# Kernel tuning notes

Hardware: AMD Instinct MI355X
Metric: run time of the kernel (lower is better)

Reference implementation:

```python
import jax, jax.numpy as jnp
import numpy as np

TEMPERATURE = 0.07
EPS = 1e-8
B, D, C = 4096, 512, 10


def setup_inputs() -> dict:
    key = jax.random.key(0)
    k1, k2 = jax.random.split(key)
    features = jax.random.normal(k1, (B, D), dtype=jnp.float32)
    cls = jax.random.randint(k2, (B,), 0, C)
    labels = jax.nn.one_hot(cls, C, dtype=jnp.float32)  # [B, C] one-hot
    return {"features": features, "labels": labels}


def reference(features, labels):
    b = features.shape[0]
    # L2-normalize rows
    feats = features / jnp.linalg.norm(features, axis=1, keepdims=True)
    sim = jnp.clip(feats @ feats.T / TEMPERATURE, -20.0, 20.0)  # [B, B]
    eye = jnp.eye(b, dtype=bool)
    sim = jnp.where(eye, -jnp.inf, sim)  # mask self-similarity

    labels_norm = labels / (labels.sum(axis=1, keepdims=True) + EPS)
    label_sim = labels_norm @ labels_norm.T  # [B, B]
    label_sim = jnp.where(eye, 0.0, label_sim)
    pos_mask = label_sim > 0.1  # [B, B] bool

    exp_sim = jnp.exp(sim)  # diag -> exp(-inf) = 0
    pos_sum = jnp.sum(jnp.where(pos_mask, exp_sim, 0.0), axis=1)  # [B]
    all_sum = jnp.sum(exp_sim, axis=1)  # diag already zero => off-diagonal sum
    loss_i = -jnp.log(pos_sum / (all_sum + EPS) + EPS)  # [B]

    valid = jnp.any(pos_mask, axis=1)  # rows with >=1 positive
    n_valid = jnp.sum(valid.astype(jnp.float32))
    total = jnp.sum(jnp.where(valid, loss_i, 0.0))
    return jnp.where(n_valid > 0, total / n_valid, 0.0)
```

## Files before the change

kernel.cpp:

```cpp
#include <hip/hip_runtime.h>


#define B_ROWS 4096
#define D_DIM  512
#define C_CLS  10
#define NTB    32
#define NTILES (NTB * (NTB + 1) / 2)

typedef __bf16 bf16x8 __attribute__((ext_vector_type(8)));
typedef float  f32x4  __attribute__((ext_vector_type(4)));

__device__ __forceinline__ void load_lds16(const __bf16* g, __bf16* l) {
  __builtin_amdgcn_global_load_lds(
      (const __attribute__((address_space(1))) unsigned int*)g,
      (__attribute__((address_space(3))) unsigned int*)l, 16, 0, 0);
}

__global__ __launch_bounds__(256) void prep_kernel(
    const float* __restrict__ feats, const float* __restrict__ labels,
    __bf16* __restrict__ F, int* __restrict__ cls,
    float* __restrict__ totals) {
  const int w = threadIdx.x >> 6, lane = threadIdx.x & 63;
  const int row = blockIdx.x * 4 + w;
  const float* fr = feats + (size_t)row * D_DIM;
  float4 v0 = ((const float4*)fr)[2 * lane];
  float4 v1 = ((const float4*)fr)[2 * lane + 1];
  float ss = v0.x*v0.x + v0.y*v0.y + v0.z*v0.z + v0.w*v0.w
           + v1.x*v1.x + v1.y*v1.y + v1.z*v1.z + v1.w*v1.w;
  #pragma unroll
  for (int m = 1; m < 64; m <<= 1) ss += __shfl_xor(ss, m, 64);
  float inv = 1.0f / sqrtf(ss);

  bf16x8 o;
  o[0] = (__bf16)(v0.x * inv); o[1] = (__bf16)(v0.y * inv);
  o[2] = (__bf16)(v0.z * inv); o[3] = (__bf16)(v0.w * inv);
  o[4] = (__bf16)(v1.x * inv); o[5] = (__bf16)(v1.y * inv);
  o[6] = (__bf16)(v1.z * inv); o[7] = (__bf16)(v1.w * inv);
  *(bf16x8*)(F + (size_t)row * D_DIM + 8 * lane) = o;

  float lv = (lane < C_CLS) ? labels[(size_t)row * C_CLS + lane] : 0.f;
  unsigned long long m = __ballot(lv > 0.5f);
  if (lane == 0) cls[row] = (int)(__ffsll((long long)m) - 1);
  if (blockIdx.x == 0 && threadIdx.x == 0) { totals[0] = 0.f; totals[1] = 0.f; }
}

__global__ __launch_bounds__(256) void sim_kernel(
    const __bf16* __restrict__ F, const int* __restrict__ cls,
    float* __restrict__ P_all, float* __restrict__ P_pos) {
  __shared__ __align__(16) __bf16 Abuf[128 * 64];
  __shared__ __align__(16) __bf16 Bbuf[128 * 64];
  __shared__ int clsA[128], clsB[128];
  __shared__ float g_row_all[128], g_row_pos[128];
  __shared__ float g_col_all[128], g_col_pos[128];

  int rem = blockIdx.x, bi = 0, rowlen = NTB;
  while (rem >= rowlen) { rem -= rowlen; ++bi; --rowlen; }
  const int bj = bi + rem;
  const int i0 = bi * 128, j0 = bj * 128;
  const bool offdiag = (bi != bj);

  const int t = threadIdx.x;
  const int w = t >> 6, lane = t & 63;
  const int wi = w & 1, wj = w >> 1;
  const int q = lane >> 4, cl = lane & 15;

  if (t < 128) { clsA[t] = cls[i0 + t]; g_row_all[t] = 0.f; g_row_pos[t] = 0.f; }
  else { clsB[t-128] = cls[j0 + t - 128]; g_col_all[t-128] = 0.f; g_col_pos[t-128] = 0.f; }

  f32x4 acc[4][4];
  #pragma unroll
  for (int ri = 0; ri < 4; ++ri)
    #pragma unroll
    for (int cj = 0; cj < 4; ++cj) acc[ri][cj] = (f32x4){0.f, 0.f, 0.f, 0.f};

  const int srow = lane >> 3;
  const int sg   = (lane & 7) ^ srow;

  for (int k0 = 0; k0 < D_DIM; k0 += 64) {
    __syncthreads();
    #pragma unroll
    for (int r = 0; r < 4; ++r) {
      const int rowbase = w * 32 + r * 8;
      load_lds16(F + (size_t)(i0 + rowbase + srow) * D_DIM + k0 + sg * 8,
                 &Abuf[rowbase * 64]);
      load_lds16(F + (size_t)(j0 + rowbase + srow) * D_DIM + k0 + sg * 8,
                 &Bbuf[rowbase * 64]);
    }
    __syncthreads();

    #pragma unroll
    for (int kk = 0; kk < 64; kk += 32) {
      const int cc = ((kk >> 3) + q) ^ (cl & 7);
      bf16x8 af[4], bfr[4];
      #pragma unroll
      for (int ri = 0; ri < 4; ++ri)
        af[ri] = *(const bf16x8*)&Abuf[(64 * wi + 16 * ri + cl) * 64 + cc * 8];
      #pragma unroll
      for (int cj = 0; cj < 4; ++cj)
        bfr[cj] = *(const bf16x8*)&Bbuf[(64 * wj + 16 * cj + cl) * 64 + cc * 8];
      #pragma unroll
      for (int ri = 0; ri < 4; ++ri)
        #pragma unroll
        for (int cj = 0; cj < 4; ++cj)
          acc[ri][cj] = __builtin_amdgcn_mfma_f32_16x16x32_bf16(
              af[ri], bfr[cj], acc[ri][cj], 0, 0, 0);
    }
  }

  const float invT = 1.0f / 0.07f;
  float cs_all[4] = {0.f, 0.f, 0.f, 0.f};
  float cs_pos[4] = {0.f, 0.f, 0.f, 0.f};

  #pragma unroll
  for (int ri = 0; ri < 4; ++ri) {
    float ra[4] = {0.f, 0.f, 0.f, 0.f};
    float rp[4] = {0.f, 0.f, 0.f, 0.f};
    #pragma unroll
    for (int cj = 0; cj < 4; ++cj) {
      const int jloc = 64 * wj + 16 * cj + cl;
      const int gj = j0 + jloc;
      const int cjc = clsB[jloc];
      #pragma unroll
      for (int r = 0; r < 4; ++r) {
        const int iloc = 64 * wi + 16 * ri + q * 4 + r;
        const int gi = i0 + iloc;
        float s = acc[ri][cj][r] * invT;
        s = fminf(fmaxf(s, -20.f), 20.f);
        const bool diag = (gi == gj);
        float e = diag ? 0.f : __expf(s);
        ra[r] += e;
        cs_all[cj] += e;
        if (!diag && cjc == clsA[iloc]) { rp[r] += e; cs_pos[cj] += e; }
      }
    }
    #pragma unroll
    for (int r = 0; r < 4; ++r) {
      float sa = ra[r], sp = rp[r];
      #pragma unroll
      for (int m = 1; m < 16; m <<= 1) {
        sa += __shfl_xor(sa, m, 64);
        sp += __shfl_xor(sp, m, 64);
      }
      if (cl == 0) {
        const int rloc = 64 * wi + 16 * ri + q * 4 + r;
        atomicAdd(&g_row_all[rloc], sa);
        atomicAdd(&g_row_pos[rloc], sp);
      }
    }
  }
  if (offdiag) {
    #pragma unroll
    for (int cj = 0; cj < 4; ++cj) {
      float sa = cs_all[cj], sp = cs_pos[cj];
      sa += __shfl_xor(sa, 16, 64); sa += __shfl_xor(sa, 32, 64);
      sp += __shfl_xor(sp, 16, 64); sp += __shfl_xor(sp, 32, 64);
      if (q == 0) {
        const int jloc = 64 * wj + 16 * cj + cl;
        atomicAdd(&g_col_all[jloc], sa);
        atomicAdd(&g_col_pos[jloc], sp);
      }
    }
  }
  __syncthreads();

  if (t < 128) {
    const size_t base_row = ((size_t)bi * NTB + bj) * 128;
    P_all[base_row + t] = g_row_all[t];
    P_pos[base_row + t] = g_row_pos[t];
  } else if (offdiag) {
    const size_t base_col = ((size_t)bj * NTB + bi) * 128;
    P_all[base_col + t - 128] = g_col_all[t - 128];
    P_pos[base_col + t - 128] = g_col_pos[t - 128];
  }
}

__global__ __launch_bounds__(256) void finalize_kernel(
    const float* __restrict__ P_all, const float* __restrict__ P_pos,
    float* __restrict__ totals) {
  __shared__ float Sall[4096], Spos[4096];
  __shared__ float redL[2], redC[2];
  const int s = blockIdx.x;
  const int t = threadIdx.x;
  for (int i = t; i < 4096; i += 256) {
    Sall[i] = P_all[(size_t)s * 4096 + i];
    Spos[i] = P_pos[(size_t)s * 4096 + i];
  }
  __syncthreads();
  if (t < 128) {
    float a = 0.f, p = 0.f;
    #pragma unroll 8
    for (int k = 0; k < 32; ++k) {
      a += Sall[k * 128 + t];
      p += Spos[k * 128 + t];
    }
    float loss = 0.f, cnt = 0.f;
    if (p > 0.f) {
      loss = -logf(p / (a + 1e-8f) + 1e-8f);
      cnt = 1.f;
    }
    #pragma unroll
    for (int m = 1; m < 64; m <<= 1) {
      loss += __shfl_xor(loss, m, 64);
      cnt  += __shfl_xor(cnt, m, 64);
    }
    if ((t & 63) == 0) { redL[t >> 6] = loss; redC[t >> 6] = cnt; }
  }
  __syncthreads();
  if (t == 0) {
    atomicAdd(&totals[0], redL[0] + redL[1]);
    atomicAdd(&totals[1], redC[0] + redC[1]);
  }
}

__global__ void div_kernel(const float* __restrict__ totals,
                           float* __restrict__ out) {
  out[0] = (totals[1] > 0.f) ? (totals[0] / totals[1]) : 0.f;
}

extern "C" void kernel_launch(void* const* d_in, const int* in_sizes, int n_in,
                              void* d_out, int out_size, void* d_ws, size_t ws_size,
                              hipStream_t stream) {
  const float* features = (const float*)d_in[0];
  const float* labels   = (const float*)d_in[1];
  float* out = (float*)d_out;

  __bf16* F      = (__bf16*)d_ws;
  int*    cls    = (int*)((char*)d_ws + (size_t)B_ROWS * D_DIM * 2);
  float*  P_all  = (float*)((char*)cls + B_ROWS * sizeof(int));
  float*  P_pos  = P_all + (size_t)NTB * NTB * 128;
  float*  totals = P_pos + (size_t)NTB * NTB * 128;

  prep_kernel<<<B_ROWS / 4, 256, 0, stream>>>(features, labels, F, cls, totals);
  sim_kernel<<<NTILES, 256, 0, stream>>>(F, cls, P_all, P_pos);
  finalize_kernel<<<NTB, 256, 0, stream>>>(P_all, P_pos, totals);
  div_kernel<<<1, 1, 0, stream>>>(totals, out);
}
```

Before: 96.56 us.

## Use 512-thread blocks with 64x32 warp tiles and register-staged LDS loads

```diff
diff --git a/kernel.cpp b/kernel.cpp
--- a/kernel.cpp
+++ b/kernel.cpp
@@ -9,12 +9,6 @@
 
 typedef __bf16 bf16x8 __attribute__((ext_vector_type(8)));
 typedef float  f32x4  __attribute__((ext_vector_type(4)));
-
-__device__ __forceinline__ void load_lds16(const __bf16* g, __bf16* l) {
-  __builtin_amdgcn_global_load_lds(
-      (const __attribute__((address_space(1))) unsigned int*)g,
-      (__attribute__((address_space(3))) unsigned int*)l, 16, 0, 0);
-}
 
 __global__ __launch_bounds__(256) void prep_kernel(
     const float* __restrict__ feats, const float* __restrict__ labels,
@@ -44,7 +38,7 @@
   if (blockIdx.x == 0 && threadIdx.x == 0) { totals[0] = 0.f; totals[1] = 0.f; }
 }
 
-__global__ __launch_bounds__(256) void sim_kernel(
+__global__ __launch_bounds__(512) void sim_kernel(
     const __bf16* __restrict__ F, const int* __restrict__ cls,
     float* __restrict__ P_all, float* __restrict__ P_pos) {
   __shared__ __align__(16) __bf16 Abuf[128 * 64];
@@ -65,59 +59,66 @@
   const int q = lane >> 4, cl = lane & 15;
 
   if (t < 128) { clsA[t] = cls[i0 + t]; g_row_all[t] = 0.f; g_row_pos[t] = 0.f; }
-  else { clsB[t-128] = cls[j0 + t - 128]; g_col_all[t-128] = 0.f; g_col_pos[t-128] = 0.f; }
-
-  f32x4 acc[4][4];
+  else if (t < 256) {
+    clsB[t-128] = cls[j0 + t - 128];
+    g_col_all[t-128] = 0.f; g_col_pos[t-128] = 0.f;
+  }
+
+  f32x4 acc[4][2];
   #pragma unroll
   for (int ri = 0; ri < 4; ++ri)
     #pragma unroll
-    for (int cj = 0; cj < 4; ++cj) acc[ri][cj] = (f32x4){0.f, 0.f, 0.f, 0.f};
-
-  const int srow = lane >> 3;
-  const int sg   = (lane & 7) ^ srow;
+    for (int cj = 0; cj < 2; ++cj) acc[ri][cj] = (f32x4){0.f, 0.f, 0.f, 0.f};
+
+  const int srow = t >> 2;
+  const int c0   = (t & 3) * 2;
+  const int sw0  = c0 ^ (srow & 7);
+  const int sw1  = (c0 + 1) ^ (srow & 7);
 
   for (int k0 = 0; k0 < D_DIM; k0 += 64) {
     __syncthreads();
-    #pragma unroll
-    for (int r = 0; r < 4; ++r) {
-      const int rowbase = w * 32 + r * 8;
-      load_lds16(F + (size_t)(i0 + rowbase + srow) * D_DIM + k0 + sg * 8,
-                 &Abuf[rowbase * 64]);
-      load_lds16(F + (size_t)(j0 + rowbase + srow) * D_DIM + k0 + sg * 8,
-                 &Bbuf[rowbase * 64]);
+    {
+      const uint4* ga = (const uint4*)(F + (size_t)(i0 + srow) * D_DIM + k0 + c0 * 8);
+      const uint4* gb = (const uint4*)(F + (size_t)(j0 + srow) * D_DIM + k0 + c0 * 8);
+      uint4 a0 = ga[0], a1 = ga[1];
+      uint4 b0 = gb[0], b1 = gb[1];
+      *(uint4*)&Abuf[srow * 64 + sw0 * 8] = a0;
+      *(uint4*)&Abuf[srow * 64 + sw1 * 8] = a1;
+      *(uint4*)&Bbuf[srow * 64 + sw0 * 8] = b0;
+      *(uint4*)&Bbuf[srow * 64 + sw1 * 8] = b1;
     }
     __syncthreads();
 
     #pragma unroll
     for (int kk = 0; kk < 64; kk += 32) {
       const int cc = ((kk >> 3) + q) ^ (cl & 7);
-      bf16x8 af[4], bfr[4];
+      bf16x8 af[4], bf[2];
       #pragma unroll
       for (int ri = 0; ri < 4; ++ri)
         af[ri] = *(const bf16x8*)&Abuf[(64 * wi + 16 * ri + cl) * 64 + cc * 8];
       #pragma unroll
-      for (int cj = 0; cj < 4; ++cj)
-        bfr[cj] = *(const bf16x8*)&Bbuf[(64 * wj + 16 * cj + cl) * 64 + cc * 8];
+      for (int cj = 0; cj < 2; ++cj)
+        bf[cj] = *(const bf16x8*)&Bbuf[(32 * wj + 16 * cj + cl) * 64 + cc * 8];
       #pragma unroll
       for (int ri = 0; ri < 4; ++ri)
         #pragma unroll
-        for (int cj = 0; cj < 4; ++cj)
+        for (int cj = 0; cj < 2; ++cj)
           acc[ri][cj] = __builtin_amdgcn_mfma_f32_16x16x32_bf16(
-              af[ri], bfr[cj], acc[ri][cj], 0, 0, 0);
+              af[ri], bf[cj], acc[ri][cj], 0, 0, 0);
     }
   }
 
   const float invT = 1.0f / 0.07f;
-  float cs_all[4] = {0.f, 0.f, 0.f, 0.f};
-  float cs_pos[4] = {0.f, 0.f, 0.f, 0.f};
+  float cs_all[2] = {0.f, 0.f};
+  float cs_pos[2] = {0.f, 0.f};
 
   #pragma unroll
   for (int ri = 0; ri < 4; ++ri) {
     float ra[4] = {0.f, 0.f, 0.f, 0.f};
     float rp[4] = {0.f, 0.f, 0.f, 0.f};
     #pragma unroll
-    for (int cj = 0; cj < 4; ++cj) {
-      const int jloc = 64 * wj + 16 * cj + cl;
+    for (int cj = 0; cj < 2; ++cj) {
+      const int jloc = 32 * wj + 16 * cj + cl;
       const int gj = j0 + jloc;
       const int cjc = clsB[jloc];
       #pragma unroll
@@ -150,12 +151,12 @@
   }
   if (offdiag) {
     #pragma unroll
-    for (int cj = 0; cj < 4; ++cj) {
+    for (int cj = 0; cj < 2; ++cj) {
       float sa = cs_all[cj], sp = cs_pos[cj];
       sa += __shfl_xor(sa, 16, 64); sa += __shfl_xor(sa, 32, 64);
       sp += __shfl_xor(sp, 16, 64); sp += __shfl_xor(sp, 32, 64);
       if (q == 0) {
-        const int jloc = 64 * wj + 16 * cj + cl;
+        const int jloc = 32 * wj + 16 * cj + cl;
         atomicAdd(&g_col_all[jloc], sa);
         atomicAdd(&g_col_pos[jloc], sp);
       }
@@ -167,7 +168,7 @@
     const size_t base_row = ((size_t)bi * NTB + bj) * 128;
     P_all[base_row + t] = g_row_all[t];
     P_pos[base_row + t] = g_row_pos[t];
-  } else if (offdiag) {
+  } else if (t < 256 && offdiag) {
     const size_t base_col = ((size_t)bj * NTB + bi) * 128;
     P_all[base_col + t - 128] = g_col_all[t - 128];
     P_pos[base_col + t - 128] = g_col_pos[t - 128];
@@ -231,7 +232,7 @@
   float*  totals = P_pos + (size_t)NTB * NTB * 128;
 
   prep_kernel<<<B_ROWS / 4, 256, 0, stream>>>(features, labels, F, cls, totals);
-  sim_kernel<<<NTILES, 256, 0, stream>>>(F, cls, P_all, P_pos);
+  sim_kernel<<<NTILES, 512, 0, stream>>>(F, cls, P_all, P_pos);
   finalize_kernel<<<NTB, 256, 0, stream>>>(P_all, P_pos, totals);
   div_kernel<<<1, 1, 0, stream>>>(totals, out);
 }
```

After: 96.53 us. About the same (-0.0%).
